# Performance work log

Measured on AMD Instinct MI355X. Metric: run time of the kernel, lower is better.

Reference implementation:

```python
import jax, jax.numpy as jnp
import numpy as np

N_NODES = 100000
N_EDGES = 3200000


def setup_inputs() -> dict:
    key = jax.random.key(0)
    ks = jax.random.split(key, 12)
    x = jax.random.normal(ks[0], (N_NODES, 34), dtype=jnp.float32)
    edge_index = jax.random.randint(ks[1], (2, N_EDGES), 0, N_NODES, dtype=jnp.int64)
    def lin(k, fin, fout):
        s = 1.0 / np.sqrt(fin)
        kw, kb = jax.random.split(k)
        W = jax.random.uniform(kw, (fin, fout), jnp.float32, -s, s)
        b = jax.random.uniform(kb, (fout,), jnp.float32, -s, s)
        return W, b
    W1, b1 = lin(ks[2], 34, 64)
    W2, b2 = lin(ks[3], 64, 32)
    W3, b3 = lin(ks[4], 32, 16)
    W4, b4 = lin(ks[5], 16, 8)
    Wc, bc = lin(ks[6], 8, 2)
    return {"x": x, "edge_index": edge_index,
            "W1": W1, "b1": b1, "W2": W2, "b2": b2,
            "W3": W3, "b3": b3, "W4": W4, "b4": b4,
            "Wc": Wc, "bc": bc}


def _gcn_norm(edge_index, n_nodes):
    # PyG GCNConv: add self-loops, symmetric normalization D^-1/2 (A+I) D^-1/2
    loop = jnp.arange(n_nodes, dtype=edge_index.dtype)
    src = jnp.concatenate([edge_index[0], loop])  # [E+N]
    dst = jnp.concatenate([edge_index[1], loop])
    deg = jax.ops.segment_sum(jnp.ones_like(dst, dtype=jnp.float32), dst,
                              num_segments=n_nodes)
    dinv = jnp.where(deg > 0, jax.lax.rsqrt(deg), 0.0)
    norm = dinv[src] * dinv[dst]  # [E+N]
    return src, dst, norm


def _gcn_conv(h, W, b, src, dst, norm, n_nodes):
    h = h @ W                                    # [N, Fout] small GEMM
    msg = h[src] * norm[:, None]                 # gather + scale
    out = jax.ops.segment_sum(msg, dst, num_segments=n_nodes)  # scatter-add
    return out + b


def reference(x, edge_index, W1, b1, W2, b2, W3, b3, W4, b4, Wc, bc):
    n = x.shape[0]
    src, dst, norm = _gcn_norm(edge_index, n)
    h = jnp.tanh(_gcn_conv(x, W1, b1, src, dst, norm, n))
    h = jnp.tanh(_gcn_conv(h, W2, b2, src, dst, norm, n))
    h = jnp.tanh(_gcn_conv(h, W3, b3, src, dst, norm, n))
    h = jnp.tanh(_gcn_conv(h, W4, b4, src, dst, norm, n))
    out = h @ Wc + bc
    return (out, h)
```

## Files before the change

kernel.cpp:

```cpp
#include <hip/hip_runtime.h>
#include <math.h>

#define N_NODES 100000
#define BSHIFT 8
#define BNODES 256
#define NB ((N_NODES + BNODES - 1) / BNODES)
#define CHUNK 8192


__device__ __forceinline__ unsigned short f2bf(float x) {
    unsigned u = __float_as_uint(x);
    u += 0x7FFFu + ((u >> 16) & 1u);
    return (unsigned short)(u >> 16);
}
__device__ __forceinline__ unsigned pack2(float a, float b) {
    return (unsigned)f2bf(a) | ((unsigned)f2bf(b) << 16);
}
__device__ __forceinline__ float bflo(unsigned u) { return __uint_as_float(u << 16); }
__device__ __forceinline__ float bfhi(unsigned u) { return __uint_as_float(u & 0xFFFF0000u); }


__global__ __launch_bounds__(256) void bucket_count(const int* __restrict__ dst,
                                                    int* __restrict__ bucketCount, int E) {
    __shared__ int hist[NB];
    for (int i = threadIdx.x; i < NB; i += 256) hist[i] = 0;
    __syncthreads();
    int i = blockIdx.x * blockDim.x + threadIdx.x;
    int stride = gridDim.x * blockDim.x;
    for (int e = i; e < E; e += stride)
        atomicAdd(&hist[dst[e] >> BSHIFT], 1);
    __syncthreads();
    for (int i2 = threadIdx.x; i2 < NB; i2 += 256) {
        int c = hist[i2];
        if (c) atomicAdd(&bucketCount[i2], c);
    }
}


__global__ __launch_bounds__(512) void bucket_scan(const int* __restrict__ bucketCount,
                                                   int* __restrict__ bucketOff,
                                                   int* __restrict__ bucketCursor, int E) {
    __shared__ int sh[512];
    int t = threadIdx.x;
    int v = (t < NB) ? bucketCount[t] : 0;
    sh[t] = v;
    __syncthreads();
    for (int d = 1; d < 512; d <<= 1) {
        int u = (t >= d) ? sh[t - d] : 0;
        __syncthreads();
        sh[t] += u;
        __syncthreads();
    }
    if (t < NB) { bucketOff[t] = sh[t] - v; bucketCursor[t] = sh[t] - v; }
    if (t == 0) bucketOff[NB] = E;
}


__global__ __launch_bounds__(256) void bucket_fill(const int* __restrict__ src,
                                                   const int* __restrict__ dst,
                                                   int* __restrict__ bucketCursor,
                                                   unsigned int* __restrict__ binned, int E) {
    __shared__ int hist[NB];
    __shared__ int base[NB];
    __shared__ int lcur[NB];
    __shared__ unsigned int recs[CHUNK];
    __shared__ unsigned short bkt[CHUNK];
    int t = threadIdx.x;
    for (int i = t; i < NB; i += 256) { hist[i] = 0; lcur[i] = 0; }
    __syncthreads();
    int cbase = blockIdx.x * CHUNK;
#pragma unroll
    for (int j = 0; j < CHUNK / 256; ++j) {
        int slot = t + j * 256;
        int e = cbase + slot;
        if (e < E) {
            int s = src[e];
            int d = dst[e];
            recs[slot] = (unsigned)s | ((unsigned)(d & (BNODES - 1)) << 17);
            int b = d >> BSHIFT;
            bkt[slot] = (unsigned short)b;
            atomicAdd(&hist[b], 1);
        } else {
            bkt[slot] = 0xFFFF;
        }
    }
    __syncthreads();
    for (int i = t; i < NB; i += 256) {
        int c = hist[i];
        base[i] = c ? atomicAdd(&bucketCursor[i], c) : 0;
    }
    __syncthreads();
#pragma unroll
    for (int j = 0; j < CHUNK / 256; ++j) {
        int slot = t + j * 256;
        unsigned short b = bkt[slot];
        if (b != 0xFFFF) {
            int pos = base[b] + atomicAdd(&lcur[b], 1);
            binned[pos] = recs[slot];
        }
    }
}


__global__ __launch_bounds__(256) void node_off_dinv(const unsigned int* __restrict__ binned,
                                                     const int* __restrict__ bucketOff,
                                                     int* __restrict__ off,
                                                     float* __restrict__ dinv, int n, int E) {
    __shared__ int hist[BNODES];
    __shared__ int sh[BNODES];
    int t = threadIdx.x;
    int b = blockIdx.x;
    hist[t] = 0;
    __syncthreads();
    int rb = bucketOff[b], re = bucketOff[b + 1];
    for (int e = rb + t; e < re; e += 256)
        atomicAdd(&hist[(binned[e] >> 17) & 255], 1);
    __syncthreads();
    int v = hist[t];
    sh[t] = v;
    __syncthreads();
    for (int d = 1; d < 256; d <<= 1) {
        int u = (t >= d) ? sh[t - d] : 0;
        __syncthreads();
        sh[t] += u;
        __syncthreads();
    }
    int g = b * BNODES + t;
    if (g < n) {
        off[g] = rb + sh[t] - v;
        dinv[g] = rsqrtf((float)v + 1.0f);
    }
    if (b == NB - 1 && t == 0) off[n] = E;
}


__global__ __launch_bounds__(256) void node_sort(const unsigned int* __restrict__ binned,
                                                 const int* __restrict__ bucketOff,
                                                 const int* __restrict__ off,
                                                 int* __restrict__ srcs, int n) {
    __shared__ int lcur[BNODES];
    int t = threadIdx.x;
    int b = blockIdx.x;
    int g = b * BNODES + t;
    lcur[t] = (g < n) ? off[g] : 0;
    __syncthreads();
    int rb = bucketOff[b], re = bucketOff[b + 1];
    for (int e = rb + t; e < re; e += 256) {
        unsigned int r = binned[e];
        int dl = (r >> 17) & 255;
        int pos = atomicAdd(&lcur[dl], 1);
        srcs[pos] = (int)(r & 0x1FFFF);
    }
}


__global__ void x_pack(const float* __restrict__ x, unsigned* __restrict__ xm,
                       unsigned* __restrict__ xt, int n) {
    int i = blockIdx.x * blockDim.x + threadIdx.x;
    if (i >= n) return;
    const float2* xr = (const float2*)(x + (size_t)i * 34);
    unsigned* om = xm + (size_t)i * 16;
#pragma unroll
    for (int j = 0; j < 16; ++j) { float2 v = xr[j]; om[j] = pack2(v.x, v.y); }
    float2 v = xr[16];
    xt[i] = pack2(v.x, v.y);
}


__global__ __launch_bounds__(256) void gather_x_bf16(const int* __restrict__ off,
        const int* __restrict__ srcs, const unsigned* __restrict__ xm,
        const unsigned* __restrict__ xt, const float* __restrict__ dinv,
        float* __restrict__ aggx, int n) {
    int g = blockIdx.x * 16 + (threadIdx.x >> 4);
    int f = threadIdx.x & 15;
    if (g >= n) return;
    int rb = off[g], re = off[g + 1];
    float dv = dinv[g];
    unsigned ug = xm[(size_t)g * 16 + f];
    float a0 = dv * dv * bflo(ug), a1 = dv * dv * bfhi(ug);
    float a2 = 0.f, a3 = 0.f;
    if (f == 0) { unsigned t = xt[g]; a2 = dv * dv * bflo(t); a3 = dv * dv * bfhi(t); }
    int e = rb;
    for (; e + 4 <= re; e += 4) {
        int s0 = srcs[e], s1 = srcs[e + 1], s2 = srcs[e + 2], s3 = srcs[e + 3];
        unsigned u0 = xm[(size_t)s0 * 16 + f], u1 = xm[(size_t)s1 * 16 + f];
        unsigned u2 = xm[(size_t)s2 * 16 + f], u3 = xm[(size_t)s3 * 16 + f];
        float w0 = dinv[s0] * dv, w1 = dinv[s1] * dv, w2 = dinv[s2] * dv, w3 = dinv[s3] * dv;
        a0 = fmaf(w0, bflo(u0), a0); a1 = fmaf(w0, bfhi(u0), a1);
        a0 = fmaf(w1, bflo(u1), a0); a1 = fmaf(w1, bfhi(u1), a1);
        a0 = fmaf(w2, bflo(u2), a0); a1 = fmaf(w2, bfhi(u2), a1);
        a0 = fmaf(w3, bflo(u3), a0); a1 = fmaf(w3, bfhi(u3), a1);
        if (f == 0) {
            unsigned t0 = xt[s0], t1 = xt[s1], t2 = xt[s2], t3 = xt[s3];
            a2 = fmaf(w0, bflo(t0), a2); a3 = fmaf(w0, bfhi(t0), a3);
            a2 = fmaf(w1, bflo(t1), a2); a3 = fmaf(w1, bfhi(t1), a3);
            a2 = fmaf(w2, bflo(t2), a2); a3 = fmaf(w2, bfhi(t2), a3);
            a2 = fmaf(w3, bflo(t3), a2); a3 = fmaf(w3, bfhi(t3), a3);
        }
    }
    for (; e < re; ++e) {
        int s = srcs[e];
        unsigned u = xm[(size_t)s * 16 + f];
        float w = dinv[s] * dv;
        a0 = fmaf(w, bflo(u), a0); a1 = fmaf(w, bfhi(u), a1);
        if (f == 0) {
            unsigned t = xt[s];
            a2 = fmaf(w, bflo(t), a2); a3 = fmaf(w, bfhi(t), a3);
        }
    }
    float2* og = (float2*)(aggx + (size_t)g * 34);
    og[f] = make_float2(a0, a1);
    if (f == 0) og[16] = make_float2(a2, a3);
}


template<int FIN, int FOUT>
__global__ void gemm_tanh(const float* __restrict__ h, const float* __restrict__ W,
                          const float* __restrict__ bias, float* __restrict__ o, int n) {
    __shared__ float sW[FIN * FOUT];
    for (int i = threadIdx.x; i < FIN * FOUT; i += blockDim.x) sW[i] = W[i];
    __syncthreads();
    constexpr int ROWS = 256 / FOUT;
    int f = threadIdx.x % FOUT;
    int r = threadIdx.x / FOUT;
    int row = blockIdx.x * ROWS + r;
    if (row >= n) return;
    const float* hr = h + (size_t)row * FIN;
    float acc = 0.f;
#pragma unroll
    for (int k = 0; k < FIN; ++k) acc = fmaf(hr[k], sW[k * FOUT + f], acc);
    o[(size_t)row * FOUT + f] = tanhf(acc + bias[f]);
}


template<int FIN, int FOUT>
__global__ void gemm_pack(const float* __restrict__ h, const float* __restrict__ W,
                          unsigned* __restrict__ linh, int n) {
    __shared__ float sW[FIN * FOUT];
    for (int i = threadIdx.x; i < FIN * FOUT; i += blockDim.x) sW[i] = W[i];
    __syncthreads();
    constexpr int NL = FOUT / 2;
    constexpr int ROWS = 256 / NL;
    int f = threadIdx.x % NL;
    int r = threadIdx.x / NL;
    int row = blockIdx.x * ROWS + r;
    if (row >= n) return;
    const float* hr = h + (size_t)row * FIN;
    float a0 = 0.f, a1 = 0.f;
#pragma unroll
    for (int k = 0; k < FIN; ++k) {
        float v = hr[k];
        a0 = fmaf(v, sW[k * FOUT + 2 * f], a0);
        a1 = fmaf(v, sW[k * FOUT + 2 * f + 1], a1);
    }
    linh[(size_t)row * NL + f] = pack2(a0, a1);
}


template<int F>
__global__ __launch_bounds__(256) void gather_bf16(const int* __restrict__ off,
        const int* __restrict__ srcs, const unsigned* __restrict__ linh,
        const float* __restrict__ dinv, const float* __restrict__ bias,
        float* __restrict__ h, int n) {
    constexpr int NL = F / 2;
    int g = blockIdx.x * (256 / NL) + threadIdx.x / NL;
    int f = threadIdx.x % NL;
    if (g >= n) return;
    int rb = off[g], re = off[g + 1];
    float dv = dinv[g];
    unsigned ug = linh[(size_t)g * NL + f];
    float a0 = dv * dv * bflo(ug), a1 = dv * dv * bfhi(ug);
    int e = rb;
    for (; e + 4 <= re; e += 4) {
        int s0 = srcs[e], s1 = srcs[e + 1], s2 = srcs[e + 2], s3 = srcs[e + 3];
        unsigned u0 = linh[(size_t)s0 * NL + f], u1 = linh[(size_t)s1 * NL + f];
        unsigned u2 = linh[(size_t)s2 * NL + f], u3 = linh[(size_t)s3 * NL + f];
        float w0 = dinv[s0] * dv, w1 = dinv[s1] * dv, w2 = dinv[s2] * dv, w3 = dinv[s3] * dv;
        a0 = fmaf(w0, bflo(u0), a0); a1 = fmaf(w0, bfhi(u0), a1);
        a0 = fmaf(w1, bflo(u1), a0); a1 = fmaf(w1, bfhi(u1), a1);
        a0 = fmaf(w2, bflo(u2), a0); a1 = fmaf(w2, bfhi(u2), a1);
        a0 = fmaf(w3, bflo(u3), a0); a1 = fmaf(w3, bfhi(u3), a1);
    }
    for (; e < re; ++e) {
        int s = srcs[e];
        unsigned u = linh[(size_t)s * NL + f];
        float w = dinv[s] * dv;
        a0 = fmaf(w, bflo(u), a0); a1 = fmaf(w, bfhi(u), a1);
    }
    a0 = tanhf(a0 + bias[2 * f]);
    a1 = tanhf(a1 + bias[2 * f + 1]);
    *(float2*)(h + (size_t)g * F + 2 * f) = make_float2(a0, a1);
}


__global__ void classifier_kernel(const float* __restrict__ h, const float* __restrict__ Wc,
                                  const float* __restrict__ bc, float* __restrict__ out, int n) {
    int i = blockIdx.x * blockDim.x + threadIdx.x;
    if (i >= n) return;
    const float* hr = h + (size_t)i * 8;
    float a0 = bc[0], a1 = bc[1];
#pragma unroll
    for (int k = 0; k < 8; ++k) {
        float v = hr[k];
        a0 = fmaf(v, Wc[k * 2 + 0], a0);
        a1 = fmaf(v, Wc[k * 2 + 1], a1);
    }
    out[(size_t)i * 2 + 0] = a0;
    out[(size_t)i * 2 + 1] = a1;
}


static inline char* alignp(char* p) {
    return (char*)(((uintptr_t)p + 15) & ~(uintptr_t)15);
}

extern "C" void kernel_launch(void* const* d_in, const int* in_sizes, int n_in,
                              void* d_out, int out_size, void* d_ws, size_t ws_size,
                              hipStream_t stream) {
    const float* x  = (const float*)d_in[0];
    const int*   ei = (const int*)d_in[1];
    const float* W1 = (const float*)d_in[2];  const float* b1 = (const float*)d_in[3];
    const float* W2 = (const float*)d_in[4];  const float* b2 = (const float*)d_in[5];
    const float* W3 = (const float*)d_in[6];  const float* b3 = (const float*)d_in[7];
    const float* W4 = (const float*)d_in[8];  const float* b4 = (const float*)d_in[9];
    const float* Wc = (const float*)d_in[10]; const float* bc = (const float*)d_in[11];

    float* out  = (float*)d_out;
    float* hout = out + (size_t)2 * N_NODES;

    const int n = N_NODES;
    const int E = in_sizes[1] / 2;
    const int* src = ei;
    const int* dst = ei + E;

    char* w = (char*)d_ws;
    float*        dinv         = (float*)w;        w = alignp(w + (size_t)n * 4);
    int*          bucketCount  = (int*)w;          w = alignp(w + (size_t)NB * 4);
    int*          bucketOff    = (int*)w;          w = alignp(w + (size_t)(NB + 1) * 4);
    int*          bucketCursor = (int*)w;          w = alignp(w + (size_t)NB * 4);
    int*          off          = (int*)w;          w = alignp(w + (size_t)(n + 1) * 4);
    unsigned int* binned       = (unsigned int*)w; w = alignp(w + (size_t)E * 4);
    int*          srcs         = (int*)w;          w = alignp(w + (size_t)E * 4);
    unsigned int* xm           = (unsigned int*)w; w = alignp(w + (size_t)n * 16 * 4);
    unsigned int* xt           = (unsigned int*)w; w = alignp(w + (size_t)n * 4);
    float*        aggx         = (float*)w;        w = alignp(w + (size_t)n * 34 * 4);
    float*        hA           = (float*)w;        w = alignp(w + (size_t)n * 64 * 4);
    float*        hB           = (float*)w;        w = alignp(w + (size_t)n * 32 * 4);
    unsigned int* linh         = (unsigned int*)w; w = alignp(w + (size_t)n * 16 * 4);

    hipMemsetAsync(bucketCount, 0, NB * sizeof(int), stream);
    bucket_count<<<1024, 256, 0, stream>>>(dst, bucketCount, E);
    bucket_scan<<<1, 512, 0, stream>>>(bucketCount, bucketOff, bucketCursor, E);
    bucket_fill<<<(E + CHUNK - 1) / CHUNK, 256, 0, stream>>>(src, dst, bucketCursor, binned, E);
    node_off_dinv<<<NB, 256, 0, stream>>>(binned, bucketOff, off, dinv, n, E);
    node_sort<<<NB, 256, 0, stream>>>(binned, bucketOff, off, srcs, n);
    x_pack<<<(n + 255) / 256, 256, 0, stream>>>(x, xm, xt, n);

    gather_x_bf16<<<(n + 15) / 16, 256, 0, stream>>>(off, srcs, xm, xt, dinv, aggx, n);
    gemm_tanh<34, 64><<<(n + 3) / 4, 256, 0, stream>>>(aggx, W1, b1, hA, n);

    gemm_pack<64, 32><<<(n + 15) / 16, 256, 0, stream>>>(hA, W2, linh, n);
    gather_bf16<32><<<(n + 15) / 16, 256, 0, stream>>>(off, srcs, linh, dinv, b2, hB, n);

    gemm_pack<32, 16><<<(n + 31) / 32, 256, 0, stream>>>(hB, W3, linh, n);
    gather_bf16<16><<<(n + 31) / 32, 256, 0, stream>>>(off, srcs, linh, dinv, b3, hA, n);

    gemm_pack<16, 8><<<(n + 63) / 64, 256, 0, stream>>>(hA, W4, linh, n);
    gather_bf16<8><<<(n + 63) / 64, 256, 0, stream>>>(off, srcs, linh, dinv, b4, hout, n);

    classifier_kernel<<<(n + 255) / 256, 256, 0, stream>>>(hout, Wc, bc, out, n);
}
```

Baseline: 498.6 us.

## Prescale features by source dinv, fuse node sort and classifier, use nontemporal accesses

Result: slower. 510.9 us (+2.5%).

```diff
diff --git a/kernel.cpp b/kernel.cpp
--- a/kernel.cpp
+++ b/kernel.cpp
@@ -8,6 +8,8 @@
 #define CHUNK 8192
 
 
+typedef float f32x2 __attribute__((ext_vector_type(2)));
+
 __device__ __forceinline__ unsigned short f2bf(float x) {
     unsigned u = __float_as_uint(x);
     u += 0x7FFFu + ((u >> 16) & 1u);
@@ -19,6 +21,13 @@
 __device__ __forceinline__ float bflo(unsigned u) { return __uint_as_float(u << 16); }
 __device__ __forceinline__ float bfhi(unsigned u) { return __uint_as_float(u & 0xFFFF0000u); }
 
+__device__ __forceinline__ int nt_ld(const int* p) { return __builtin_nontemporal_load(p); }
+__device__ __forceinline__ void nt_st2(float* p, float a, float b) {
+    f32x2 v; v.x = a; v.y = b;
+    __builtin_nontemporal_store(v, (f32x2*)p);
+}
+__device__ __forceinline__ void nt_st(float* p, float a) { __builtin_nontemporal_store(a, p); }
+
 
 __global__ __launch_bounds__(256) void bucket_count(const int* __restrict__ dst,
                                                     int* __restrict__ bucketCount, int E) {
@@ -28,7 +37,7 @@
     int i = blockIdx.x * blockDim.x + threadIdx.x;
     int stride = gridDim.x * blockDim.x;
     for (int e = i; e < E; e += stride)
-        atomicAdd(&hist[dst[e] >> BSHIFT], 1);
+        atomicAdd(&hist[nt_ld(dst + e) >> BSHIFT], 1);
     __syncthreads();
     for (int i2 = threadIdx.x; i2 < NB; i2 += 256) {
         int c = hist[i2];
@@ -74,8 +83,8 @@
         int slot = t + j * 256;
         int e = cbase + slot;
         if (e < E) {
-            int s = src[e];
-            int d = dst[e];
+            int s = nt_ld(src + e);
+            int d = nt_ld(dst + e);
             recs[slot] = (unsigned)s | ((unsigned)(d & (BNODES - 1)) << 17);
             int b = d >> BSHIFT;
             bkt[slot] = (unsigned short)b;
@@ -102,12 +111,14 @@
 }
 
 
-__global__ __launch_bounds__(256) void node_off_dinv(const unsigned int* __restrict__ binned,
+__global__ __launch_bounds__(256) void node_off_sort(const unsigned int* __restrict__ binned,
                                                      const int* __restrict__ bucketOff,
                                                      int* __restrict__ off,
-                                                     float* __restrict__ dinv, int n, int E) {
+                                                     float* __restrict__ dinv,
+                                                     int* __restrict__ srcs, int n, int E) {
     __shared__ int hist[BNODES];
     __shared__ int sh[BNODES];
+    __shared__ int lcur[BNODES];
     int t = threadIdx.x;
     int b = blockIdx.x;
     hist[t] = 0;
@@ -125,45 +136,34 @@
         sh[t] += u;
         __syncthreads();
     }
+    int base = rb + sh[t] - v;
+    lcur[t] = base;
     int g = b * BNODES + t;
     if (g < n) {
-        off[g] = rb + sh[t] - v;
+        off[g] = base;
         dinv[g] = rsqrtf((float)v + 1.0f);
     }
     if (b == NB - 1 && t == 0) off[n] = E;
-}
-
-
-__global__ __launch_bounds__(256) void node_sort(const unsigned int* __restrict__ binned,
-                                                 const int* __restrict__ bucketOff,
-                                                 const int* __restrict__ off,
-                                                 int* __restrict__ srcs, int n) {
-    __shared__ int lcur[BNODES];
-    int t = threadIdx.x;
-    int b = blockIdx.x;
-    int g = b * BNODES + t;
-    lcur[t] = (g < n) ? off[g] : 0;
-    __syncthreads();
-    int rb = bucketOff[b], re = bucketOff[b + 1];
+    __syncthreads();
     for (int e = rb + t; e < re; e += 256) {
         unsigned int r = binned[e];
-        int dl = (r >> 17) & 255;
-        int pos = atomicAdd(&lcur[dl], 1);
+        int pos = atomicAdd(&lcur[(r >> 17) & 255], 1);
         srcs[pos] = (int)(r & 0x1FFFF);
     }
 }
 
 
-__global__ void x_pack(const float* __restrict__ x, unsigned* __restrict__ xm,
-                       unsigned* __restrict__ xt, int n) {
+__global__ void x_pack(const float* __restrict__ x, const float* __restrict__ dinv,
+                       unsigned* __restrict__ xm, unsigned* __restrict__ xt, int n) {
     int i = blockIdx.x * blockDim.x + threadIdx.x;
     if (i >= n) return;
+    float dv = dinv[i];
     const float2* xr = (const float2*)(x + (size_t)i * 34);
     unsigned* om = xm + (size_t)i * 16;
 #pragma unroll
-    for (int j = 0; j < 16; ++j) { float2 v = xr[j]; om[j] = pack2(v.x, v.y); }
+    for (int j = 0; j < 16; ++j) { float2 v = xr[j]; om[j] = pack2(dv * v.x, dv * v.y); }
     float2 v = xr[16];
-    xt[i] = pack2(v.x, v.y);
+    xt[i] = pack2(dv * v.x, dv * v.y);
 }
 
 
@@ -175,42 +175,42 @@
     int f = threadIdx.x & 15;
     if (g >= n) return;
     int rb = off[g], re = off[g + 1];
-    float dv = dinv[g];
     unsigned ug = xm[(size_t)g * 16 + f];
-    float a0 = dv * dv * bflo(ug), a1 = dv * dv * bfhi(ug);
+    float a0 = bflo(ug), a1 = bfhi(ug);
     float a2 = 0.f, a3 = 0.f;
-    if (f == 0) { unsigned t = xt[g]; a2 = dv * dv * bflo(t); a3 = dv * dv * bfhi(t); }
+    if (f == 0) { unsigned tt = xt[g]; a2 = bflo(tt); a3 = bfhi(tt); }
     int e = rb;
-    for (; e + 4 <= re; e += 4) {
-        int s0 = srcs[e], s1 = srcs[e + 1], s2 = srcs[e + 2], s3 = srcs[e + 3];
+    for (; e + 8 <= re; e += 8) {
+        int s0 = nt_ld(srcs + e),     s1 = nt_ld(srcs + e + 1);
+        int s2 = nt_ld(srcs + e + 2), s3 = nt_ld(srcs + e + 3);
+        int s4 = nt_ld(srcs + e + 4), s5 = nt_ld(srcs + e + 5);
+        int s6 = nt_ld(srcs + e + 6), s7 = nt_ld(srcs + e + 7);
         unsigned u0 = xm[(size_t)s0 * 16 + f], u1 = xm[(size_t)s1 * 16 + f];
         unsigned u2 = xm[(size_t)s2 * 16 + f], u3 = xm[(size_t)s3 * 16 + f];
-        float w0 = dinv[s0] * dv, w1 = dinv[s1] * dv, w2 = dinv[s2] * dv, w3 = dinv[s3] * dv;
-        a0 = fmaf(w0, bflo(u0), a0); a1 = fmaf(w0, bfhi(u0), a1);
-        a0 = fmaf(w1, bflo(u1), a0); a1 = fmaf(w1, bfhi(u1), a1);
-        a0 = fmaf(w2, bflo(u2), a0); a1 = fmaf(w2, bfhi(u2), a1);
-        a0 = fmaf(w3, bflo(u3), a0); a1 = fmaf(w3, bfhi(u3), a1);
+        unsigned u4 = xm[(size_t)s4 * 16 + f], u5 = xm[(size_t)s5 * 16 + f];
+        unsigned u6 = xm[(size_t)s6 * 16 + f], u7 = xm[(size_t)s7 * 16 + f];
+        a0 += bflo(u0); a1 += bfhi(u0); a0 += bflo(u1); a1 += bfhi(u1);
+        a0 += bflo(u2); a1 += bfhi(u2); a0 += bflo(u3); a1 += bfhi(u3);
+        a0 += bflo(u4); a1 += bfhi(u4); a0 += bflo(u5); a1 += bfhi(u5);
+        a0 += bflo(u6); a1 += bfhi(u6); a0 += bflo(u7); a1 += bfhi(u7);
         if (f == 0) {
             unsigned t0 = xt[s0], t1 = xt[s1], t2 = xt[s2], t3 = xt[s3];
-            a2 = fmaf(w0, bflo(t0), a2); a3 = fmaf(w0, bfhi(t0), a3);
-            a2 = fmaf(w1, bflo(t1), a2); a3 = fmaf(w1, bfhi(t1), a3);
-            a2 = fmaf(w2, bflo(t2), a2); a3 = fmaf(w2, bfhi(t2), a3);
-            a2 = fmaf(w3, bflo(t3), a2); a3 = fmaf(w3, bfhi(t3), a3);
+            unsigned t4 = xt[s4], t5 = xt[s5], t6 = xt[s6], t7 = xt[s7];
+            a2 += bflo(t0); a3 += bfhi(t0); a2 += bflo(t1); a3 += bfhi(t1);
+            a2 += bflo(t2); a3 += bfhi(t2); a2 += bflo(t3); a3 += bfhi(t3);
+            a2 += bflo(t4); a3 += bfhi(t4); a2 += bflo(t5); a3 += bfhi(t5);
+            a2 += bflo(t6); a3 += bfhi(t6); a2 += bflo(t7); a3 += bfhi(t7);
         }
     }
     for (; e < re; ++e) {
-        int s = srcs[e];
+        int s = nt_ld(srcs + e);
         unsigned u = xm[(size_t)s * 16 + f];
-        float w = dinv[s] * dv;
-        a0 = fmaf(w, bflo(u), a0); a1 = fmaf(w, bfhi(u), a1);
-        if (f == 0) {
-            unsigned t = xt[s];
-            a2 = fmaf(w, bflo(t), a2); a3 = fmaf(w, bfhi(t), a3);
-        }
-    }
-    float2* og = (float2*)(aggx + (size_t)g * 34);
-    og[f] = make_float2(a0, a1);
-    if (f == 0) og[16] = make_float2(a2, a3);
+        a0 += bflo(u); a1 += bfhi(u);
+        if (f == 0) { unsigned tt = xt[s]; a2 += bflo(tt); a3 += bfhi(tt); }
+    }
+    float dv = dinv[g];
+    nt_st2(aggx + (size_t)g * 34 + 2 * f, dv * a0, dv * a1);
+    if (f == 0) nt_st2(aggx + (size_t)g * 34 + 32, dv * a2, dv * a3);
 }
 
 
@@ -229,13 +229,13 @@
     float acc = 0.f;
 #pragma unroll
     for (int k = 0; k < FIN; ++k) acc = fmaf(hr[k], sW[k * FOUT + f], acc);
-    o[(size_t)row * FOUT + f] = tanhf(acc + bias[f]);
+    nt_st(o + (size_t)row * FOUT + f, tanhf(acc + bias[f]));
 }
 
 
 template<int FIN, int FOUT>
 __global__ void gemm_pack(const float* __restrict__ h, const float* __restrict__ W,
-                          unsigned* __restrict__ linh, int n) {
+                          const float* __restrict__ dinv, unsigned* __restrict__ linh, int n) {
     __shared__ float sW[FIN * FOUT];
     for (int i = threadIdx.x; i < FIN * FOUT; i += blockDim.x) sW[i] = W[i];
     __syncthreads();
@@ -253,60 +253,58 @@
         a0 = fmaf(v, sW[k * FOUT + 2 * f], a0);
         a1 = fmaf(v, sW[k * FOUT + 2 * f + 1], a1);
     }
-    linh[(size_t)row * NL + f] = pack2(a0, a1);
-}
-
-
-template<int F>
+    float dv = dinv[row];
+    linh[(size_t)row * NL + f] = pack2(dv * a0, dv * a1);
+}
+
+
+template<int F, bool CLS>
 __global__ __launch_bounds__(256) void gather_bf16(const int* __restrict__ off,
         const int* __restrict__ srcs, const unsigned* __restrict__ linh,
         const float* __restrict__ dinv, const float* __restrict__ bias,
-        float* __restrict__ h, int n) {
+        float* __restrict__ h, const float* __restrict__ Wc,
+        const float* __restrict__ bc, float* __restrict__ out, int n) {
     constexpr int NL = F / 2;
     int g = blockIdx.x * (256 / NL) + threadIdx.x / NL;
     int f = threadIdx.x % NL;
     if (g >= n) return;
     int rb = off[g], re = off[g + 1];
-    float dv = dinv[g];
     unsigned ug = linh[(size_t)g * NL + f];
-    float a0 = dv * dv * bflo(ug), a1 = dv * dv * bfhi(ug);
+    float a0 = bflo(ug), a1 = bfhi(ug);
     int e = rb;
-    for (; e + 4 <= re; e += 4) {
-        int s0 = srcs[e], s1 = srcs[e + 1], s2 = srcs[e + 2], s3 = srcs[e + 3];
+    for (; e + 8 <= re; e += 8) {
+        int s0 = nt_ld(srcs + e),     s1 = nt_ld(srcs + e + 1);
+        int s2 = nt_ld(srcs + e + 2), s3 = nt_ld(srcs + e + 3);
+        int s4 = nt_ld(srcs + e + 4), s5 = nt_ld(srcs + e + 5);
+        int s6 = nt_ld(srcs + e + 6), s7 = nt_ld(srcs + e + 7);
         unsigned u0 = linh[(size_t)s0 * NL + f], u1 = linh[(size_t)s1 * NL + f];
         unsigned u2 = linh[(size_t)s2 * NL + f], u3 = linh[(size_t)s3 * NL + f];
-        float w0 = dinv[s0] * dv, w1 = dinv[s1] * dv, w2 = dinv[s2] * dv, w3 = dinv[s3] * dv;
-        a0 = fmaf(w0, bflo(u0), a0); a1 = fmaf(w0, bfhi(u0), a1);
-        a0 = fmaf(w1, bflo(u1), a0); a1 = fmaf(w1, bfhi(u1), a1);
-        a0 = fmaf(w2, bflo(u2), a0); a1 = fmaf(w2, bfhi(u2), a1);
-        a0 = fmaf(w3, bflo(u3), a0); a1 = fmaf(w3, bfhi(u3), a1);
+        unsigned u4 = linh[(size_t)s4 * NL + f], u5 = linh[(size_t)s5 * NL + f];
+        unsigned u6 = linh[(size_t)s6 * NL + f], u7 = linh[(size_t)s7 * NL + f];
+        a0 += bflo(u0); a1 += bfhi(u0); a0 += bflo(u1); a1 += bfhi(u1);
+        a0 += bflo(u2); a1 += bfhi(u2); a0 += bflo(u3); a1 += bfhi(u3);
+        a0 += bflo(u4); a1 += bfhi(u4); a0 += bflo(u5); a1 += bfhi(u5);
+        a0 += bflo(u6); a1 += bfhi(u6); a0 += bflo(u7); a1 += bfhi(u7);
     }
     for (; e < re; ++e) {
-        int s = srcs[e];
+        int s = nt_ld(srcs + e);
         unsigned u = linh[(size_t)s * NL + f];
-        float w = dinv[s] * dv;
-        a0 = fmaf(w, bflo(u), a0); a1 = fmaf(w, bfhi(u), a1);
-    }
-    a0 = tanhf(a0 + bias[2 * f]);
-    a1 = tanhf(a1 + bias[2 * f + 1]);
-    *(float2*)(h + (size_t)g * F + 2 * f) = make_float2(a0, a1);
-}
-
-
-__global__ void classifier_kernel(const float* __restrict__ h, const float* __restrict__ Wc,
-                                  const float* __restrict__ bc, float* __restrict__ out, int n) {
-    int i = blockIdx.x * blockDim.x + threadIdx.x;
-    if (i >= n) return;
-    const float* hr = h + (size_t)i * 8;
-    float a0 = bc[0], a1 = bc[1];
-#pragma unroll
-    for (int k = 0; k < 8; ++k) {
-        float v = hr[k];
-        a0 = fmaf(v, Wc[k * 2 + 0], a0);
-        a1 = fmaf(v, Wc[k * 2 + 1], a1);
-    }
-    out[(size_t)i * 2 + 0] = a0;
-    out[(size_t)i * 2 + 1] = a1;
+        a0 += bflo(u); a1 += bfhi(u);
+    }
+    float dv = dinv[g];
+    a0 = tanhf(fmaf(dv, a0, bias[2 * f]));
+    a1 = tanhf(fmaf(dv, a1, bias[2 * f + 1]));
+    nt_st2(h + (size_t)g * F + 2 * f, a0, a1);
+    if (CLS) {
+        float p0 = a0 * Wc[4 * f]     + a1 * Wc[4 * f + 2];
+        float p1 = a0 * Wc[4 * f + 1] + a1 * Wc[4 * f + 3];
+        p0 += __shfl_xor(p0, 1); p1 += __shfl_xor(p1, 1);
+        p0 += __shfl_xor(p0, 2); p1 += __shfl_xor(p1, 2);
+        if (f == 0) {
+            out[(size_t)g * 2]     = p0 + bc[0];
+            out[(size_t)g * 2 + 1] = p1 + bc[1];
+        }
+    }
 }
 
 
@@ -352,21 +350,21 @@
     bucket_count<<<1024, 256, 0, stream>>>(dst, bucketCount, E);
     bucket_scan<<<1, 512, 0, stream>>>(bucketCount, bucketOff, bucketCursor, E);
     bucket_fill<<<(E + CHUNK - 1) / CHUNK, 256, 0, stream>>>(src, dst, bucketCursor, binned, E);
-    node_off_dinv<<<NB, 256, 0, stream>>>(binned, bucketOff, off, dinv, n, E);
-    node_sort<<<NB, 256, 0, stream>>>(binned, bucketOff, off, srcs, n);
-    x_pack<<<(n + 255) / 256, 256, 0, stream>>>(x, xm, xt, n);
+    node_off_sort<<<NB, 256, 0, stream>>>(binned, bucketOff, off, dinv, srcs, n, E);
+    x_pack<<<(n + 255) / 256, 256, 0, stream>>>(x, dinv, xm, xt, n);
 
     gather_x_bf16<<<(n + 15) / 16, 256, 0, stream>>>(off, srcs, xm, xt, dinv, aggx, n);
     gemm_tanh<34, 64><<<(n + 3) / 4, 256, 0, stream>>>(aggx, W1, b1, hA, n);
 
-    gemm_pack<64, 32><<<(n + 15) / 16, 256, 0, stream>>>(hA, W2, linh, n);
-    gather_bf16<32><<<(n + 15) / 16, 256, 0, stream>>>(off, srcs, linh, dinv, b2, hB, n);
-
-    gemm_pack<32, 16><<<(n + 31) / 32, 256, 0, stream>>>(hB, W3, linh, n);
-    gather_bf16<16><<<(n + 31) / 32, 256, 0, stream>>>(off, srcs, linh, dinv, b3, hA, n);
-
-    gemm_pack<16, 8><<<(n + 63) / 64, 256, 0, stream>>>(hA, W4, linh, n);
-    gather_bf16<8><<<(n + 63) / 64, 256, 0, stream>>>(off, srcs, linh, dinv, b4, hout, n);
-
-    classifier_kernel<<<(n + 255) / 256, 256, 0, stream>>>(hout, Wc, bc, out, n);
-}
+    gemm_pack<64, 32><<<(n + 15) / 16, 256, 0, stream>>>(hA, W2, dinv, linh, n);
+    gather_bf16<32, false><<<(n + 15) / 16, 256, 0, stream>>>(off, srcs, linh, dinv, b2, hB,
+                                                              Wc, bc, out, n);
+
+    gemm_pack<32, 16><<<(n + 31) / 32, 256, 0, stream>>>(hB, W3, dinv, linh, n);
+    gather_bf16<16, false><<<(n + 31) / 32, 256, 0, stream>>>(off, srcs, linh, dinv, b3, hA,
+                                                              Wc, bc, out, n);
+
+    gemm_pack<16, 8><<<(n + 63) / 64, 256, 0, stream>>>(hA, W4, dinv, linh, n);
+    gather_bf16<8, true><<<(n + 63) / 64, 256, 0, stream>>>(off, srcs, linh, dinv, b4, hout,
+                                                            Wc, bc, out, n);
+}
```
